# Kernel optimization log

Measured on AMD Instinct MI355X. Metric: run time of the kernel, lower is better.

Reference implementation:

```python
import jax, jax.numpy as jnp
import numpy as np

IN_FEATURES = 2048
OUT_FEATURES = 65536
RANK = 64
ALPHA = 128
SCALING = ALPHA / RANK


def setup_inputs() -> dict:
    key = jax.random.key(0)
    k_x, k_w, k_a, k_b = jax.random.split(key, 4)
    x = jax.random.normal(k_x, (1, 2048, IN_FEATURES), dtype=jnp.float32)
    # weight: [out, in]  (kaiming-uniform in torch; normal*scale is fine for a numeric baseline)
    weight = jax.random.normal(k_w, (OUT_FEATURES, IN_FEATURES), dtype=jnp.float32) * (1.0 / np.sqrt(IN_FEATURES))
    lora_A = jax.random.normal(k_a, (RANK, IN_FEATURES), dtype=jnp.float32) * (1.0 / np.sqrt(IN_FEATURES))
    # lora_B is zero-initialized in the module; use small random values so the LoRA branch is exercised
    lora_B = jax.random.normal(k_b, (OUT_FEATURES, RANK), dtype=jnp.float32) * 0.01
    return {"x": x, "weight": weight, "lora_A": lora_A, "lora_B": lora_B}


def reference(x, weight, lora_A, lora_B):
    # F.linear(x, W) + scaling * F.linear(F.linear(x, lora_A), lora_B)
    # base: [B,T,in] @ [in,out] -> [B,T,out]
    base = jnp.einsum("btc,vc->btv", x, weight)
    low = jnp.einsum("btc,rc->btr", x, lora_A)        # [B,T,r]
    lora = jnp.einsum("btr,vr->btv", low, lora_B)      # [B,T,out]
    return base + SCALING * lora
```

## Files before the change

### kernel.cpp

```cpp
#include <hip/hip_runtime.h>
#include <hip/hip_bf16.h>
#include <stdint.h>
#include <stddef.h>


#define IN_F   2048
#define OUT_F  65536
#define RANK   64
#define M_TOK  2048
#define KP     2112

#define BM 128
#define BN 128
#define BK 32
#define BROW 40

typedef __attribute__((ext_vector_type(8))) short    short8;
typedef __attribute__((ext_vector_type(4))) float    float4v;
typedef __attribute__((ext_vector_type(4))) unsigned short ushort4v;
typedef __attribute__((ext_vector_type(8))) unsigned short ushort8v;

__device__ __forceinline__ unsigned short f2bf(float f) {
  union { float f; unsigned u; } v; v.f = f;
  return (unsigned short)((v.u + 0x7FFFu + ((v.u >> 16) & 1u)) >> 16);
}

__device__ __forceinline__ void gload_lds16(const void* g, void* l) {
  __builtin_amdgcn_global_load_lds(
      (const __attribute__((address_space(1))) unsigned int*)g,
      (__attribute__((address_space(3))) unsigned int*)l, 16, 0, 0);
}

__global__ void cvt_x_kernel(const float* __restrict__ x, unsigned short* __restrict__ xp) {
  const int row = blockIdx.x;
  const int c   = threadIdx.x * 8;
  const float4v* s = (const float4v*)(x + (size_t)row * IN_F + c);
  float4v a = s[0], b = s[1];
  ushort8v o;
  o[0] = f2bf(a.x); o[1] = f2bf(a.y); o[2] = f2bf(a.z); o[3] = f2bf(a.w);
  o[4] = f2bf(b.x); o[5] = f2bf(b.y); o[6] = f2bf(b.z); o[7] = f2bf(b.w);
  *(ushort8v*)(xp + (size_t)row * KP + c) = o;
}

__global__ void low_kernel(const float* __restrict__ x, const float* __restrict__ A,
                           unsigned short* __restrict__ xp) {
  __shared__ float xs[128 * 8];
  __shared__ float as_[128 * 64];
  const int t  = threadIdx.x;
  const int m0 = blockIdx.x * 8;
  const int r  = t & 63;
  const int mg = t >> 6;
  float acc0 = 0.f, acc1 = 0.f;
  for (int k0 = 0; k0 < IN_F; k0 += 128) {
    __syncthreads();
    {
      const int m = t >> 5, kq = (t & 31) * 4;
      float4v v = *(const float4v*)(x + (size_t)(m0 + m) * IN_F + k0 + kq);
      xs[(kq + 0) * 8 + m] = v.x; xs[(kq + 1) * 8 + m] = v.y;
      xs[(kq + 2) * 8 + m] = v.z; xs[(kq + 3) * 8 + m] = v.w;
    }
#pragma unroll
    for (int j = 0; j < 8; ++j) {
      const int f = t + 256 * j;
      const int rr = f >> 5, q = f & 31;
      float4v v = *(const float4v*)(A + (size_t)rr * IN_F + k0 + q * 4);
      as_[(q * 4 + 0) * 64 + rr] = v.x; as_[(q * 4 + 1) * 64 + rr] = v.y;
      as_[(q * 4 + 2) * 64 + rr] = v.z; as_[(q * 4 + 3) * 64 + rr] = v.w;
    }
    __syncthreads();
    const int ma = mg * 2;
#pragma unroll 8
    for (int k = 0; k < 128; ++k) {
      float a = as_[k * 64 + r];
      acc0 += a * xs[k * 8 + ma];
      acc1 += a * xs[k * 8 + ma + 1];
    }
  }
  const int ma = mg * 2;
  xp[(size_t)(m0 + ma) * KP + IN_F + r]     = f2bf(2.0f * acc0);
  xp[(size_t)(m0 + ma + 1) * KP + IN_F + r] = f2bf(2.0f * acc1);
}

__global__ void gemm_kernel(const unsigned short* __restrict__ xp,
                            const float* __restrict__ W,
                            const float* __restrict__ Bl,
                            float* __restrict__ C) {
  __shared__ __align__(16) unsigned short As[BM * BK];
  __shared__ __align__(16) unsigned short Bs[BN * BROW];

  const int t    = threadIdx.x;
  const int lane = t & 63;
  const int wid  = t >> 6;
  const int wr   = wid >> 1;
  const int wc   = wid & 1;
  const int tm   = lane & 15;
  const int quad = lane >> 4;

  const int m0 = blockIdx.x * BM;
  const int n0 = blockIdx.y * BN;

  float4v acc[4][4] = {};

  for (int k0 = 0; k0 < KP; k0 += BK) {
    __syncthreads();
    {
      const int f0 = t, f1 = t + 256;
      gload_lds16(xp + (size_t)(m0 + (f0 >> 2)) * KP + k0 + (f0 & 3) * 8, &As[f0 * 8]);
      gload_lds16(xp + (size_t)(m0 + (f1 >> 2)) * KP + k0 + (f1 & 3) * 8, &As[f1 * 8]);
    }
    const float* Bsrc; int rstride, kk;
    if (k0 < IN_F) { Bsrc = W;  rstride = IN_F; kk = k0; }
    else           { Bsrc = Bl; rstride = RANK; kk = k0 - IN_F; }
#pragma unroll
    for (int j = 0; j < 4; ++j) {
      const int f = t + 256 * j;
      const int row = f >> 3, seg = f & 7;
      float4v v = *(const float4v*)(Bsrc + (size_t)(n0 + row) * rstride + kk + seg * 4);
      ushort4v o;
      o.x = f2bf(v.x); o.y = f2bf(v.y); o.z = f2bf(v.z); o.w = f2bf(v.w);
      *(ushort4v*)&Bs[row * BROW + seg * 4] = o;
    }
    __syncthreads();
    short8 af[4], bfr[4];
#pragma unroll
    for (int i = 0; i < 4; ++i)
      af[i] = *(const short8*)&As[(wr * 64 + i * 16 + tm) * BK + quad * 8];
#pragma unroll
    for (int i = 0; i < 4; ++i)
      bfr[i] = *(const short8*)&Bs[(wc * 64 + i * 16 + tm) * BROW + quad * 8];
#pragma unroll
    for (int i = 0; i < 4; ++i)
#pragma unroll
      for (int jn = 0; jn < 4; ++jn)
        acc[i][jn] = __builtin_amdgcn_mfma_f32_16x16x32_bf16(af[i], bfr[jn], acc[i][jn], 0, 0, 0);
  }

#pragma unroll
  for (int i = 0; i < 4; ++i) {
    const int mrow = m0 + wr * 64 + i * 16 + quad * 4;
#pragma unroll
    for (int jn = 0; jn < 4; ++jn) {
      const int ncol = n0 + wc * 64 + jn * 16 + tm;
      float4v v = acc[i][jn];
      C[(size_t)(mrow + 0) * OUT_F + ncol] = v.x;
      C[(size_t)(mrow + 1) * OUT_F + ncol] = v.y;
      C[(size_t)(mrow + 2) * OUT_F + ncol] = v.z;
      C[(size_t)(mrow + 3) * OUT_F + ncol] = v.w;
    }
  }
}

extern "C" void kernel_launch(void* const* d_in, const int* in_sizes, int n_in,
                              void* d_out, int out_size, void* d_ws, size_t ws_size,
                              hipStream_t stream) {
  const float* x  = (const float*)d_in[0];
  const float* W  = (const float*)d_in[1];
  const float* lA = (const float*)d_in[2];
  const float* lB = (const float*)d_in[3];
  float* out = (float*)d_out;
  unsigned short* xp = (unsigned short*)d_ws;

  hipLaunchKernelGGL(cvt_x_kernel, dim3(M_TOK), dim3(256), 0, stream, x, xp);
  hipLaunchKernelGGL(low_kernel, dim3(M_TOK / 8), dim3(256), 0, stream, x, lA, xp);
  hipLaunchKernelGGL(gemm_kernel, dim3(M_TOK / BM, OUT_F / BN), dim3(256), 0, stream,
                     xp, W, lB, out);
}
```

Before: 1.693 ms.

## Rewrite GEMM with 256x256 tiles, double-buffered swizzled LDS, and register prefetch

The main GEMM moves to 256x256x64 tiles with 512 threads. It double-buffers A (direct global-to-LDS) and B (prefetched into registers, then converted to bf16 with the hardware cast), uses XOR-swizzled LDS layouts to avoid bank conflicts, and applies a grouped block swizzle for L2 reuse. It also uses setprio and phased barriers around the MFMA bursts. The low-rank kernel is rewritten to one row per block with a four-way split-K reduction. The larger tiles cut redundant W reads and hide load latency, at the cost of higher register and LDS pressure and much more complex synchronisation.

```diff
diff --git a/kernel.cpp b/kernel.cpp
--- a/kernel.cpp
+++ b/kernel.cpp
@@ -9,20 +9,26 @@
 #define RANK   64
 #define M_TOK  2048
 #define KP     2112
-
-#define BM 128
-#define BN 128
-#define BK 32
-#define BROW 40
-
-typedef __attribute__((ext_vector_type(8))) short    short8;
-typedef __attribute__((ext_vector_type(4))) float    float4v;
+#define NT     33
+
+#define BM 256
+#define BN 256
+#define BK 64
+#define THREADS 512
+
+typedef __attribute__((ext_vector_type(8))) short          short8;
+typedef __attribute__((ext_vector_type(4))) float          float4v;
 typedef __attribute__((ext_vector_type(4))) unsigned short ushort4v;
 typedef __attribute__((ext_vector_type(8))) unsigned short ushort8v;
 
 __device__ __forceinline__ unsigned short f2bf(float f) {
   union { float f; unsigned u; } v; v.f = f;
   return (unsigned short)((v.u + 0x7FFFu + ((v.u >> 16) & 1u)) >> 16);
+}
+
+__device__ __forceinline__ unsigned short f2bf_hw(float f) {
+  __bf16 h = (__bf16)f;
+  return __builtin_bit_cast(unsigned short, h);
 }
 
 __device__ __forceinline__ void gload_lds16(const void* g, void* l) {
@@ -44,104 +50,174 @@
 
 __global__ void low_kernel(const float* __restrict__ x, const float* __restrict__ A,
                            unsigned short* __restrict__ xp) {
-  __shared__ float xs[128 * 8];
-  __shared__ float as_[128 * 64];
-  const int t  = threadIdx.x;
-  const int m0 = blockIdx.x * 8;
-  const int r  = t & 63;
-  const int mg = t >> 6;
-  float acc0 = 0.f, acc1 = 0.f;
-  for (int k0 = 0; k0 < IN_F; k0 += 128) {
-    __syncthreads();
-    {
-      const int m = t >> 5, kq = (t & 31) * 4;
-      float4v v = *(const float4v*)(x + (size_t)(m0 + m) * IN_F + k0 + kq);
-      xs[(kq + 0) * 8 + m] = v.x; xs[(kq + 1) * 8 + m] = v.y;
-      xs[(kq + 2) * 8 + m] = v.z; xs[(kq + 3) * 8 + m] = v.w;
-    }
-#pragma unroll
-    for (int j = 0; j < 8; ++j) {
-      const int f = t + 256 * j;
-      const int rr = f >> 5, q = f & 31;
-      float4v v = *(const float4v*)(A + (size_t)rr * IN_F + k0 + q * 4);
-      as_[(q * 4 + 0) * 64 + rr] = v.x; as_[(q * 4 + 1) * 64 + rr] = v.y;
-      as_[(q * 4 + 2) * 64 + rr] = v.z; as_[(q * 4 + 3) * 64 + rr] = v.w;
-    }
-    __syncthreads();
-    const int ma = mg * 2;
+  __shared__ float xrow[IN_F];
+  __shared__ float part[4][RANK];
+  const int row = blockIdx.x;
+  const int t   = threadIdx.x;
+  {
+    const float4v* s = (const float4v*)(x + (size_t)row * IN_F);
+    float4v a = s[t * 2], b = s[t * 2 + 1];
+    *(float4v*)&xrow[t * 8]     = a;
+    *(float4v*)&xrow[t * 8 + 4] = b;
+  }
+  __syncthreads();
+  const int r = t & 63;
+  const int q = t >> 6;
+  const float* ap = A + (size_t)r * IN_F + q * 512;
+  const float* xq = xrow + q * 512;
+  float acc = 0.f;
 #pragma unroll 8
-    for (int k = 0; k < 128; ++k) {
-      float a = as_[k * 64 + r];
-      acc0 += a * xs[k * 8 + ma];
-      acc1 += a * xs[k * 8 + ma + 1];
-    }
-  }
-  const int ma = mg * 2;
-  xp[(size_t)(m0 + ma) * KP + IN_F + r]     = f2bf(2.0f * acc0);
-  xp[(size_t)(m0 + ma + 1) * KP + IN_F + r] = f2bf(2.0f * acc1);
-}
-
-__global__ void gemm_kernel(const unsigned short* __restrict__ xp,
-                            const float* __restrict__ W,
-                            const float* __restrict__ Bl,
-                            float* __restrict__ C) {
-  __shared__ __align__(16) unsigned short As[BM * BK];
-  __shared__ __align__(16) unsigned short Bs[BN * BROW];
+  for (int k = 0; k < 512; k += 4) {
+    float4v a = *(const float4v*)(ap + k);
+    acc += a.x * xq[k] + a.y * xq[k + 1] + a.z * xq[k + 2] + a.w * xq[k + 3];
+  }
+  part[q][r] = acc;
+  __syncthreads();
+  if (t < RANK) {
+    float s = part[0][t] + part[1][t] + part[2][t] + part[3][t];
+    xp[(size_t)row * KP + IN_F + t] = f2bf(2.0f * s);
+  }
+}
+
+__global__ __launch_bounds__(THREADS, 2) void gemm_kernel(
+    const unsigned short* __restrict__ xp, const float* __restrict__ W,
+    const float* __restrict__ Bl, float* __restrict__ C) {
+  __shared__ __align__(16) unsigned short As[2][BM * BK];
+  __shared__ __align__(16) unsigned short Bs[2][BN * BK];
 
   const int t    = threadIdx.x;
   const int lane = t & 63;
-  const int wid  = t >> 6;
-  const int wr   = wid >> 1;
-  const int wc   = wid & 1;
   const int tm   = lane & 15;
   const int quad = lane >> 4;
-
-  const int m0 = blockIdx.x * BM;
-  const int n0 = blockIdx.y * BN;
-
-  float4v acc[4][4] = {};
-
-  for (int k0 = 0; k0 < KP; k0 += BK) {
-    __syncthreads();
-    {
-      const int f0 = t, f1 = t + 256;
-      gload_lds16(xp + (size_t)(m0 + (f0 >> 2)) * KP + k0 + (f0 & 3) * 8, &As[f0 * 8]);
-      gload_lds16(xp + (size_t)(m0 + (f1 >> 2)) * KP + k0 + (f1 & 3) * 8, &As[f1 * 8]);
-    }
-    const float* Bsrc; int rstride, kk;
-    if (k0 < IN_F) { Bsrc = W;  rstride = IN_F; kk = k0; }
-    else           { Bsrc = Bl; rstride = RANK; kk = k0 - IN_F; }
+  const int wid  = t >> 6;
+  const int wr   = wid >> 2;
+  const int wc   = wid & 3;
+
+  const int wg  = blockIdx.x;
+  const int swz = (wg & 7) * (2048 / 8) + (wg >> 3);
+  const int m0  = (swz & 7) * BM;
+  const int n0  = (swz >> 3) * BN;
+
+  const int s7   = tm & 7;
+  const int sw0  = ((0 + quad) ^ s7) << 3;
+  const int sw1  = ((4 + quad) ^ s7) << 3;
+  const int aOff = (wr * 128 + tm) * BK;
+  const int bOff = (wc * 64 + tm) * BK;
+
+  float4v acc[8][4] = {};
+  float4v breg[8];
+
+  auto stageA = [&](int kt, int buf) {
+#pragma unroll
+    for (int i = 0; i < 4; ++i) {
+      const int f = i * 512 + t;
+      const int row = f >> 3, sl = f & 7;
+      const unsigned short* src =
+          xp + (size_t)(m0 + row) * KP + kt * BK + ((sl ^ (row & 7)) << 3);
+      gload_lds16(src, &As[buf][f * 8]);
+    }
+  };
+
+  auto loadB = [&](int kt) {
+    const float* src; int rs, ko;
+    if (kt < 32) { src = W;  rs = IN_F; ko = kt * BK; }
+    else         { src = Bl; rs = RANK; ko = 0; }
+#pragma unroll
+    for (int j = 0; j < 8; ++j) {
+      const int f = j * 512 + t;
+      const int row = f >> 4, seg = f & 15;
+      const float* p = src + (size_t)(n0 + row) * rs + ko + seg * 4;
+      asm volatile("global_load_dwordx4 %0, %1, off" : "=v"(breg[j]) : "v"(p));
+    }
+  };
+
+  auto writeB = [&](int buf) {
+#pragma unroll
+    for (int j = 0; j < 8; ++j) {
+      const int f = j * 512 + t;
+      const int row = f >> 4, seg = f & 15;
+      ushort4v o;
+      o[0] = f2bf_hw(breg[j].x); o[1] = f2bf_hw(breg[j].y);
+      o[2] = f2bf_hw(breg[j].z); o[3] = f2bf_hw(breg[j].w);
+      const int eoff = row * BK + (((seg >> 1) ^ (row & 7)) << 3) + ((seg & 1) << 2);
+      *(ushort4v*)&Bs[buf][eoff] = o;
+    }
+  };
+
+  stageA(0, 0);
+  loadB(0);
+  asm volatile("s_waitcnt vmcnt(0)" ::: "memory");
+  __builtin_amdgcn_sched_barrier(0);
+  writeB(0);
+  loadB(1);
+  stageA(1, 1);
+  asm volatile("s_waitcnt lgkmcnt(0)" ::: "memory");
+  __builtin_amdgcn_sched_barrier(0);
+  __builtin_amdgcn_s_barrier();
+
+  for (int kt = 0; kt < NT; ++kt) {
+    const int c = kt & 1;
+    const unsigned short* ab = &As[c][0];
+    const unsigned short* bb = &Bs[c][0];
+    short8 a0[4][2], bfr[2][2];
+#pragma unroll
+    for (int p = 0; p < 4; ++p) {
+      const int mh = p >> 1;
+      const int nh = (p == 1 || p == 2) ? 1 : 0;
+      if (p == 0 || p == 2) {
+#pragma unroll
+        for (int ii = 0; ii < 4; ++ii) {
+          const int ro = aOff + (mh * 4 + ii) * 16 * BK;
+          a0[ii][0] = *(const short8*)&ab[ro + sw0];
+          a0[ii][1] = *(const short8*)&ab[ro + sw1];
+        }
+      }
+      if (p != 2) {
+#pragma unroll
+        for (int jj = 0; jj < 2; ++jj) {
+          const int ro = bOff + (nh * 2 + jj) * 16 * BK;
+          bfr[jj][0] = *(const short8*)&bb[ro + sw0];
+          bfr[jj][1] = *(const short8*)&bb[ro + sw1];
+        }
+      }
+      __builtin_amdgcn_s_barrier();
+      asm volatile("s_waitcnt lgkmcnt(0)" ::: "memory");
+      __builtin_amdgcn_sched_barrier(0);
+      __builtin_amdgcn_s_setprio(1);
+#pragma unroll
+      for (int ii = 0; ii < 4; ++ii)
+#pragma unroll
+        for (int jj = 0; jj < 2; ++jj) {
+          acc[mh * 4 + ii][nh * 2 + jj] = __builtin_amdgcn_mfma_f32_16x16x32_bf16(
+              a0[ii][0], bfr[jj][0], acc[mh * 4 + ii][nh * 2 + jj], 0, 0, 0);
+          acc[mh * 4 + ii][nh * 2 + jj] = __builtin_amdgcn_mfma_f32_16x16x32_bf16(
+              a0[ii][1], bfr[jj][1], acc[mh * 4 + ii][nh * 2 + jj], 0, 0, 0);
+        }
+      __builtin_amdgcn_s_setprio(0);
+      __builtin_amdgcn_s_barrier();
+      __builtin_amdgcn_sched_barrier(0);
+    }
+
+    if (kt == NT - 1) break;
+    asm volatile("s_waitcnt vmcnt(0)" ::: "memory");
+    __builtin_amdgcn_sched_barrier(0);
+    writeB(c ^ 1);
+    if (kt + 2 < NT) {
+      loadB(kt + 2);
+      stageA(kt + 2, c);
+    }
+    asm volatile("s_waitcnt lgkmcnt(0)" ::: "memory");
+    __builtin_amdgcn_sched_barrier(0);
+    __builtin_amdgcn_s_barrier();
+  }
+
+#pragma unroll
+  for (int i = 0; i < 8; ++i) {
+    const int mrow = m0 + wr * 128 + i * 16 + quad * 4;
 #pragma unroll
     for (int j = 0; j < 4; ++j) {
-      const int f = t + 256 * j;
-      const int row = f >> 3, seg = f & 7;
-      float4v v = *(const float4v*)(Bsrc + (size_t)(n0 + row) * rstride + kk + seg * 4);
-      ushort4v o;
-      o.x = f2bf(v.x); o.y = f2bf(v.y); o.z = f2bf(v.z); o.w = f2bf(v.w);
-      *(ushort4v*)&Bs[row * BROW + seg * 4] = o;
-    }
-    __syncthreads();
-    short8 af[4], bfr[4];
-#pragma unroll
-    for (int i = 0; i < 4; ++i)
-      af[i] = *(const short8*)&As[(wr * 64 + i * 16 + tm) * BK + quad * 8];
-#pragma unroll
-    for (int i = 0; i < 4; ++i)
-      bfr[i] = *(const short8*)&Bs[(wc * 64 + i * 16 + tm) * BROW + quad * 8];
-#pragma unroll
-    for (int i = 0; i < 4; ++i)
-#pragma unroll
-      for (int jn = 0; jn < 4; ++jn)
-        acc[i][jn] = __builtin_amdgcn_mfma_f32_16x16x32_bf16(af[i], bfr[jn], acc[i][jn], 0, 0, 0);
-  }
-
-#pragma unroll
-  for (int i = 0; i < 4; ++i) {
-    const int mrow = m0 + wr * 64 + i * 16 + quad * 4;
-#pragma unroll
-    for (int jn = 0; jn < 4; ++jn) {
-      const int ncol = n0 + wc * 64 + jn * 16 + tm;
-      float4v v = acc[i][jn];
+      const int ncol = n0 + wc * 64 + j * 16 + tm;
+      float4v v = acc[i][j];
       C[(size_t)(mrow + 0) * OUT_F + ncol] = v.x;
       C[(size_t)(mrow + 1) * OUT_F + ncol] = v.y;
       C[(size_t)(mrow + 2) * OUT_F + ncol] = v.z;
@@ -161,7 +237,7 @@
   unsigned short* xp = (unsigned short*)d_ws;
 
   hipLaunchKernelGGL(cvt_x_kernel, dim3(M_TOK), dim3(256), 0, stream, x, xp);
-  hipLaunchKernelGGL(low_kernel, dim3(M_TOK / 8), dim3(256), 0, stream, x, lA, xp);
-  hipLaunchKernelGGL(gemm_kernel, dim3(M_TOK / BM, OUT_F / BN), dim3(256), 0, stream,
+  hipLaunchKernelGGL(low_kernel, dim3(M_TOK), dim3(256), 0, stream, x, lA, xp);
+  hipLaunchKernelGGL(gemm_kernel, dim3(2048), dim3(THREADS), 0, stream,
                      xp, W, lB, out);
 }
```

Result: slower. 1.879 ms (+11.0%).
